# Performance work log

Hardware: AMD Instinct MI355X
Metric: run time of the kernel (lower is better)

Reference implementation:

```python
import jax, jax.numpy as jnp
import numpy as np

EMBED_DIM = 512
NUM_HEADS = 8
HEAD_DIM = EMBED_DIM // NUM_HEADS
B, S = 2, 4096


def setup_inputs() -> dict:
    key = jax.random.key(0)
    ks = jax.random.split(key, 5)
    scale = 1.0 / np.sqrt(EMBED_DIM)
    x = jax.random.normal(ks[0], (B, S, EMBED_DIM), dtype=jnp.float32)
    Wq = jax.random.normal(ks[1], (EMBED_DIM, EMBED_DIM), dtype=jnp.float32) * scale
    Wk = jax.random.normal(ks[2], (EMBED_DIM, EMBED_DIM), dtype=jnp.float32) * scale
    Wv = jax.random.normal(ks[3], (EMBED_DIM, EMBED_DIM), dtype=jnp.float32) * scale
    Wo = jax.random.normal(ks[4], (EMBED_DIM, EMBED_DIM), dtype=jnp.float32) * scale
    z = jnp.zeros((EMBED_DIM,), dtype=jnp.float32)
    return {"x": x, "Wq": Wq, "bq": z, "Wk": Wk, "bk": z, "Wv": Wv, "bv": z, "Wo": Wo, "bo": z}


def _split_heads(t):
    # [B, S, E] -> [B, H, S, Dh]
    b, s, _ = t.shape
    return t.reshape(b, s, NUM_HEADS, HEAD_DIM).transpose(0, 2, 1, 3)


def reference(x, Wq, bq, Wk, bk, Wv, bv, Wo, bo):
    q = _split_heads(x @ Wq + bq)
    k = _split_heads(x @ Wk + bk)
    v = _split_heads(x @ Wv + bv)
    # scaled dot-product attention; scale by sqrt(d_head) as in source
    scores = jnp.einsum("bhqd,bhkd->bhqk", q, k) / jnp.sqrt(jnp.float32(HEAD_DIM))
    weights = jax.nn.softmax(scores, axis=-1)
    attn = jnp.einsum("bhqk,bhkd->bhqd", weights, v)
    concat = attn.transpose(0, 2, 1, 3).reshape(x.shape[0], x.shape[1], EMBED_DIM)
    return concat @ Wo + bo
```

## Files before the change

### kernel.cpp

```cpp
#include <hip/hip_runtime.h>
#include <stdint.h>


typedef __bf16 bf16_t;
typedef bf16_t bf16x8 __attribute__((ext_vector_type(8)));
typedef float f32x4 __attribute__((ext_vector_type(4)));
typedef unsigned short u16;
typedef unsigned int u32;

__device__ __forceinline__ u16 f2bf(float f) {
  return __builtin_bit_cast(u16, (bf16_t)f);
}

__device__ __forceinline__ void gll16(const void* g, void* l) {
  __builtin_amdgcn_global_load_lds((__attribute__((address_space(1))) void*)(void*)(g),
                                   (__attribute__((address_space(3))) void*)(l), 16, 0, 0);
}

__device__ __forceinline__ float fexp2(float x) {
  float r; asm("v_exp_f32 %0, %1" : "=v"(r) : "v"(x)); return r;
}
__device__ __forceinline__ u32 cvtpk(float lo, float hi) {
  u32 r; asm("v_cvt_pk_bf16_f32 %0, %1, %2" : "=v"(r) : "v"(lo), "v"(hi)); return r;
}

__global__ void k_convert(const float* __restrict__ x, u16* __restrict__ xb, int n4) {
  int i = blockIdx.x * blockDim.x + threadIdx.x;
  if (i >= n4) return;
  float4 v = ((const float4*)x)[i];
  ushort4 o;
  o.x = f2bf(v.x); o.y = f2bf(v.y); o.z = f2bf(v.z); o.w = f2bf(v.w);
  ((ushort4*)xb)[i] = o;
}

__global__ void k_transposeW(const float* __restrict__ W0, const float* __restrict__ W1,
                             const float* __restrict__ W2, const float* __restrict__ W3,
                             u16* __restrict__ Wt) {
  __shared__ float tile[64][65];
  const float* W = (blockIdx.z == 0) ? W0 : (blockIdx.z == 1) ? W1 : (blockIdx.z == 2) ? W2 : W3;
  u16* out = Wt + (size_t)blockIdx.z * (512 * 512);
  int k0 = blockIdx.x * 64, n0 = blockIdx.y * 64;
  int t = threadIdx.x;
#pragma unroll
  for (int i = 0; i < 16; ++i) {
    int idx = i * 256 + t;
    int r = idx >> 6, c = idx & 63;
    tile[r][c] = W[(size_t)(k0 + r) * 512 + n0 + c];
  }
  __syncthreads();
#pragma unroll
  for (int i = 0; i < 16; ++i) {
    int idx = i * 256 + t;
    int n = idx >> 6, k = idx & 63;
    out[(size_t)(n0 + n) * 512 + k0 + k] = f2bf(tile[k][n]);
  }
}

__device__ __forceinline__ void gemm_core(const u16* __restrict__ A, const u16* __restrict__ Bt,
                                          int m0, int n0, uint8_t* lds, f32x4 (&acc)[4][4]) {
  int t = threadIdx.x;
  int lane = t & 63;
  int wid = t >> 6;
  int l15 = lane & 15, hib = (lane >> 4) * 16;
  int wm = wid >> 1, wn = wid & 1;
  const uint8_t* Ab = (const uint8_t*)A + (size_t)m0 * 1024;
  const uint8_t* Bb = (const uint8_t*)Bt + (size_t)n0 * 1024;

  auto STAGE = [&](int buf, int kk) {
    int kof = kk * 128;
    uint8_t* Al = lds + buf * 32768;
    uint8_t* Bl = Al + 16384;
#pragma unroll
    for (int r = 0; r < 4; ++r) {
      int L = r * 4096 + t * 16;
      int row = L >> 7;
      int colU = (L & 127) ^ ((row & 7) << 4);
      gll16(Ab + (size_t)row * 1024 + kof + colU, Al + L);
      gll16(Bb + (size_t)row * 1024 + kof + colU, Bl + L);
    }
  };

  STAGE(0, 0);
  asm volatile("s_waitcnt vmcnt(0)" ::: "memory");
  __builtin_amdgcn_s_barrier();

  int cur = 0;
  for (int kk = 0; kk < 8; ++kk) {
    if (kk + 1 < 8) STAGE(cur ^ 1, kk + 1);
    const uint8_t* Al = lds + cur * 32768;
    const uint8_t* Bl = Al + 16384;
#pragma unroll
    for (int ks = 0; ks < 2; ++ks) {
      bf16x8 af[4], bfr[4];
#pragma unroll
      for (int mi = 0; mi < 4; ++mi) {
        int row = wm * 64 + mi * 16 + l15;
        af[mi] = *(const bf16x8*)(Al + row * 128 + ((ks * 64 + hib) ^ ((row & 7) << 4)));
      }
#pragma unroll
      for (int ni = 0; ni < 4; ++ni) {
        int row = wn * 64 + ni * 16 + l15;
        bfr[ni] = *(const bf16x8*)(Bl + row * 128 + ((ks * 64 + hib) ^ ((row & 7) << 4)));
      }
#pragma unroll
      for (int mi = 0; mi < 4; ++mi)
#pragma unroll
        for (int ni = 0; ni < 4; ++ni)
          acc[mi][ni] = __builtin_amdgcn_mfma_f32_16x16x32_bf16(af[mi], bfr[ni], acc[mi][ni], 0, 0, 0);
    }
    asm volatile("s_waitcnt vmcnt(0)" ::: "memory");
    __builtin_amdgcn_s_barrier();
    cur ^= 1;
  }
}

__global__ __launch_bounds__(256, 2) void k_gemm_qkv(
    const u16* __restrict__ A, const u16* __restrict__ Wt,
    const float* __restrict__ bq, const float* __restrict__ bk, const float* __restrict__ bv,
    u16* __restrict__ Qo, u16* __restrict__ Ko, u16* __restrict__ Vt) {
  __shared__ uint8_t lds[65536];
  int z = blockIdx.z;
  const u16* Bt = Wt + (size_t)z * (512 * 512);
  const float* bias = (z == 0) ? bq : (z == 1) ? bk : bv;
  float qsc = (z == 0) ? 0.18033688011112042f : 1.0f;
  int m0 = blockIdx.y * 128, n0 = blockIdx.x * 128;
  int t = threadIdx.x, lane = t & 63, wid = t >> 6;
  int l15 = lane & 15;
  int wm = wid >> 1, wn = wid & 1;

  f32x4 acc[4][4] = {};
  gemm_core(A, Bt, m0, n0, lds, acc);

  if (z != 2) {
    u16* out = (z == 0) ? Qo : Ko;
#pragma unroll
    for (int mi = 0; mi < 4; ++mi)
#pragma unroll
      for (int ni = 0; ni < 4; ++ni) {
        int c = wn * 64 + ni * 16 + l15;
        float bsv = bias[n0 + c];
        int rbase = wm * 64 + mi * 16 + (lane >> 4) * 4;
#pragma unroll
        for (int i = 0; i < 4; ++i)
          *(u16*)(lds + (rbase + i) * 256 + c * 2) = f2bf((acc[mi][ni][i] + bsv) * qsc);
      }
    __syncthreads();
#pragma unroll
    for (int rr = 0; rr < 8; ++rr) {
      int L = rr * 4096 + t * 16;
      int row = L >> 8, col = L & 255;
      *(uint4*)((uint8_t*)out + (size_t)(m0 + row) * 1024 + n0 * 2 + col) = *(const uint4*)(lds + L);
    }
  } else {
#pragma unroll
    for (int mi = 0; mi < 4; ++mi)
#pragma unroll
      for (int ni = 0; ni < 4; ++ni) {
        int c = wn * 64 + ni * 16 + l15;
        float bsv = bias[n0 + c];
        int rbase = wm * 64 + mi * 16 + (lane >> 4) * 4;
#pragma unroll
        for (int i = 0; i < 4; ++i)
          *(u16*)(lds + c * 272 + (rbase + i) * 2) = f2bf(acc[mi][ni][i] + bsv);
      }
    __syncthreads();
    int b = m0 >> 12, s0 = m0 & 4095;
#pragma unroll
    for (int rr = 0; rr < 8; ++rr) {
      int L = rr * 4096 + t * 16;
      int cidx = L >> 8, rb = L & 255;
      *(uint4*)((uint8_t*)Vt + (size_t)(b * 512 + n0 + cidx) * 8192 + s0 * 2 + rb) =
          *(const uint4*)(lds + cidx * 272 + rb);
    }
  }
}

__global__ __launch_bounds__(256, 2) void k_gemm_out(
    const u16* __restrict__ A, const u16* __restrict__ Bt,
    const float* __restrict__ bias, float* __restrict__ out) {
  __shared__ uint8_t lds[65536];
  int m0 = blockIdx.y * 128, n0 = blockIdx.x * 128;
  int t = threadIdx.x, lane = t & 63, wid = t >> 6;
  int l15 = lane & 15;
  int wm = wid >> 1, wn = wid & 1;

  f32x4 acc[4][4] = {};
  gemm_core(A, Bt, m0, n0, lds, acc);

#pragma unroll
  for (int mi = 0; mi < 4; ++mi)
#pragma unroll
    for (int ni = 0; ni < 4; ++ni) {
      int c = wn * 64 + ni * 16 + l15;
      float bsv = bias[n0 + c];
      int rbase = wm * 64 + mi * 16 + (lane >> 4) * 4;
#pragma unroll
      for (int i = 0; i < 4; ++i)
        out[(size_t)(m0 + rbase + i) * 512 + n0 + c] = acc[mi][ni][i] + bsv;
    }
}

__global__ __launch_bounds__(256, 2) void k_attn(
    const u16* __restrict__ Q, const u16* __restrict__ K,
    const u16* __restrict__ Vt, u16* __restrict__ O) {
  __shared__ uint8_t lds[65536];
  int t = threadIdx.x, lane = t & 63, wid = t >> 6;
  int l15 = lane & 15, hi = lane >> 4;
  int g = wid >> 1, p = wid & 1;
  int bh = blockIdx.y, b = bh >> 3, h = bh & 7;
  int q0 = blockIdx.x * 128 + g * 64;

  const uint8_t* Kbase = (const uint8_t*)K + (size_t)(b * 4096) * 1024 + h * 128;
  const uint8_t* Vbase = (const uint8_t*)Vt + (size_t)(b * 512 + h * 64) * 8192;

  bf16x8 qf[4][2];
#pragma unroll
  for (int qs = 0; qs < 4; ++qs)
#pragma unroll
    for (int ks = 0; ks < 2; ++ks)
      qf[qs][ks] = *(const bf16x8*)(Q + (size_t)(b * 4096 + q0 + qs * 16 + l15) * 512 +
                                    h * 64 + ks * 32 + hi * 8);

  uint4 ou; ou.x = 0x3F803F80u; ou.y = 0x3F803F80u; ou.z = 0x3F803F80u; ou.w = 0x3F803F80u;
  const bf16x8 ones = __builtin_bit_cast(bf16x8, ou);

  f32x4 o[4][4] = {};
  f32x4 oden[4] = {};

  auto STAGE = [&](int buf, int kt2) {
    uint8_t* Kl = lds + buf * 32768;
    uint8_t* Vl = Kl + 16384;
    int kv0 = kt2 * 128;
#pragma unroll
    for (int r = 0; r < 4; ++r) {
      int L = r * 4096 + t * 16;
      int rowK = L >> 7;
      int colK = (L & 127) ^ ((rowK & 7) << 4);
      gll16(Kbase + (size_t)(kv0 + rowK) * 1024 + colK, Kl + L);
      int rowV = (L >> 7) & 63, sub = L >> 13;
      int colV = (L & 127) ^ ((rowV & 7) << 4);
      gll16(Vbase + (size_t)rowV * 8192 + (size_t)(kv0 + sub * 64) * 2 + colV, Vl + L);
    }
  };

  STAGE(0, 0);
  asm volatile("s_waitcnt vmcnt(0)" ::: "memory");
  __builtin_amdgcn_s_barrier();

  int cur = 0;
  for (int kt2 = 0; kt2 < 32; ++kt2) {
    if (kt2 + 1 < 32) STAGE(cur ^ 1, kt2 + 1);

    uint8_t* Kbuf = lds + cur * 32768;
    uint8_t* Vbuf = Kbuf + 16384;

#pragma unroll
    for (int sub = 0; sub < 2; ++sub) {
      const uint8_t* Kl = Kbuf + sub * 8192;
      const uint8_t* Vl = Vbuf + sub * 8192;

      bf16x8 kA[2][2];
#pragma unroll
      for (int ks = 0; ks < 2; ++ks)
#pragma unroll
        for (int cg = 0; cg < 2; ++cg) {
          int row = p * 32 + cg * 16 + l15;
          kA[ks][cg] = *(const bf16x8*)(Kl + row * 128 + ((ks * 64 + hi * 16) ^ ((row & 7) << 4)));
        }

      f32x4 s[4][2] = {};
      __builtin_amdgcn_s_setprio(1);
#pragma unroll
      for (int qs = 0; qs < 4; ++qs)
#pragma unroll
        for (int ks = 0; ks < 2; ++ks)
#pragma unroll
          for (int cg = 0; cg < 2; ++cg)
            s[qs][cg] = __builtin_amdgcn_mfma_f32_16x16x32_bf16(kA[ks][cg], qf[qs][ks], s[qs][cg], 0, 0, 0);
      __builtin_amdgcn_s_setprio(0);

      bf16x8 pb[4];
#pragma unroll
      for (int qs = 0; qs < 4; ++qs) {
        float pv[8];
#pragma unroll
        for (int cg = 0; cg < 2; ++cg)
#pragma unroll
          for (int i = 0; i < 4; ++i)
            pv[cg * 4 + i] = fexp2(s[qs][cg][i]);
        uint4 pu;
        pu.x = cvtpk(pv[0], pv[1]);
        pu.y = cvtpk(pv[2], pv[3]);
        pu.z = cvtpk(pv[4], pv[5]);
        pu.w = cvtpk(pv[6], pv[7]);
        pb[qs] = __builtin_bit_cast(bf16x8, pu);
      }

      __builtin_amdgcn_s_setprio(1);
#pragma unroll
      for (int qs = 0; qs < 4; ++qs)
        oden[qs] = __builtin_amdgcn_mfma_f32_16x16x32_bf16(ones, pb[qs], oden[qs], 0, 0, 0);
#pragma unroll
      for (int dg = 0; dg < 4; ++dg) {
        int row = dg * 16 + l15;
        int sw = (row & 7) << 4;
        uint2 a0 = *(const uint2*)(Vl + row * 128 + ((p * 64 + hi * 8) ^ sw));
        uint2 a1 = *(const uint2*)(Vl + row * 128 + ((p * 64 + 32 + hi * 8) ^ sw));
        uint4 vv; vv.x = a0.x; vv.y = a0.y; vv.z = a1.x; vv.w = a1.y;
        bf16x8 va = __builtin_bit_cast(bf16x8, vv);
#pragma unroll
        for (int qs = 0; qs < 4; ++qs)
          o[qs][dg] = __builtin_amdgcn_mfma_f32_16x16x32_bf16(va, pb[qs], o[qs][dg], 0, 0, 0);
      }
      __builtin_amdgcn_s_setprio(0);
    }

    asm volatile("s_waitcnt vmcnt(0)" ::: "memory");
    __builtin_amdgcn_s_barrier();
    cur ^= 1;
  }

  float den[4];
#pragma unroll
  for (int qs = 0; qs < 4; ++qs) den[qs] = oden[qs][0];

  uint8_t* base = lds + g * 17408;
  if (p) {
#pragma unroll
    for (int qs = 0; qs < 4; ++qs) {
#pragma unroll
      for (int dg = 0; dg < 4; ++dg)
        *(f32x4*)(base + ((qs * 4 + dg) * 64 + lane) * 16) = o[qs][dg];
      *(float*)(base + 16384 + (qs * 64 + lane) * 4) = den[qs];
    }
  }
  __syncthreads();
  if (!p) {
#pragma unroll
    for (int qs = 0; qs < 4; ++qs) {
      float pl = *(const float*)(base + 16384 + (qs * 64 + lane) * 4);
      float inv = 1.0f / (den[qs] + pl);
#pragma unroll
      for (int dg = 0; dg < 4; ++dg) {
        f32x4 po = *(const f32x4*)(base + ((qs * 4 + dg) * 64 + lane) * 16);
        ushort4 pk;
        pk.x = f2bf((o[qs][dg][0] + po[0]) * inv);
        pk.y = f2bf((o[qs][dg][1] + po[1]) * inv);
        pk.z = f2bf((o[qs][dg][2] + po[2]) * inv);
        pk.w = f2bf((o[qs][dg][3] + po[3]) * inv);
        *(uint2*)(O + (size_t)(b * 4096 + q0 + qs * 16 + l15) * 512 + h * 64 + dg * 16 + hi * 4) =
            __builtin_bit_cast(uint2, pk);
      }
    }
  }
}

extern "C" void kernel_launch(void* const* d_in, const int* in_sizes, int n_in,
                              void* d_out, int out_size, void* d_ws, size_t ws_size,
                              hipStream_t stream) {
  const float* x  = (const float*)d_in[0];
  const float* Wq = (const float*)d_in[1];
  const float* bq = (const float*)d_in[2];
  const float* Wk = (const float*)d_in[3];
  const float* bk = (const float*)d_in[4];
  const float* Wv = (const float*)d_in[5];
  const float* bv = (const float*)d_in[6];
  const float* Wo = (const float*)d_in[7];
  const float* bo = (const float*)d_in[8];
  float* out = (float*)d_out;

  uint8_t* ws = (uint8_t*)d_ws;
  u16* xb  = (u16*)(ws);
  u16* Wt  = (u16*)(ws + 8388608);
  u16* Qb  = (u16*)(ws + 10485760);
  u16* Kb  = (u16*)(ws + 18874368);
  u16* Vtb = (u16*)(ws + 27262976);
  u16* attn = xb;

  k_convert<<<4096, 256, 0, stream>>>(x, xb, 1048576);
  k_transposeW<<<dim3(8, 8, 4), 256, 0, stream>>>(Wq, Wk, Wv, Wo, Wt);
  k_gemm_qkv<<<dim3(4, 64, 3), 256, 0, stream>>>(xb, Wt, bq, bk, bv, Qb, Kb, Vtb);
  k_attn<<<dim3(32, 16), 256, 0, stream>>>(Qb, Kb, Vtb, attn);
  k_gemm_out<<<dim3(4, 64), 256, 0, stream>>>(attn, Wt + 3 * 262144, bo, out);
}
```

Before: 114.8 us.

## Split KV across four waves per 64-query block and load V directly from global

The attention kernel now gives each block 64 queries, and its four waves split each 128-key tile into 32-key slices. Only K is staged in LDS, which halves LDS use and raises the launch-bounds occupancy target to three blocks per CU. V is read straight from global memory in a permuted sequence order, and the QKV GEMM writes V^T with a matching position permutation so each lane's 8 contiguous values line up with the MFMA P layout. The four partial outputs are combined by a serial chain of LDS reductions across waves. The trade-offs are more global V traffic without LDS reuse and extra barriers in the epilogue, in exchange for more blocks and better occupancy.

```diff
diff --git a/kernel.cpp b/kernel.cpp
--- a/kernel.cpp
+++ b/kernel.cpp
@@ -160,8 +160,12 @@
         float bsv = bias[n0 + c];
         int rbase = wm * 64 + mi * 16 + (lane >> 4) * 4;
 #pragma unroll
-        for (int i = 0; i < 4; ++i)
-          *(u16*)(lds + c * 272 + (rbase + i) * 2) = f2bf(acc[mi][ni][i] + bsv);
+        for (int i = 0; i < 4; ++i) {
+          int sl = rbase + i;
+          int t5 = sl & 31;
+          int pos = (sl & ~31) | (t5 & 3) | (((t5 >> 4) & 1) << 2) | (((t5 >> 2) & 3) << 3);
+          *(u16*)(lds + c * 272 + pos * 2) = f2bf(acc[mi][ni][i] + bsv);
+        }
       }
     __syncthreads();
     int b = m0 >> 12, s0 = m0 & 4095;
@@ -200,15 +204,15 @@
     }
 }
 
-__global__ __launch_bounds__(256, 2) void k_attn(
+__global__ __launch_bounds__(256, 3) void k_attn(
     const u16* __restrict__ Q, const u16* __restrict__ K,
     const u16* __restrict__ Vt, u16* __restrict__ O) {
-  __shared__ uint8_t lds[65536];
+  __shared__ uint8_t lds[32768];
   int t = threadIdx.x, lane = t & 63, wid = t >> 6;
   int l15 = lane & 15, hi = lane >> 4;
-  int g = wid >> 1, p = wid & 1;
+  int p = wid;
   int bh = blockIdx.y, b = bh >> 3, h = bh & 7;
-  int q0 = blockIdx.x * 128 + g * 64;
+  int q0 = blockIdx.x * 64;
 
   const uint8_t* Kbase = (const uint8_t*)K + (size_t)(b * 4096) * 1024 + h * 128;
   const uint8_t* Vbase = (const uint8_t*)Vt + (size_t)(b * 512 + h * 64) * 8192;
@@ -228,18 +232,14 @@
   f32x4 oden[4] = {};
 
   auto STAGE = [&](int buf, int kt2) {
-    uint8_t* Kl = lds + buf * 32768;
-    uint8_t* Vl = Kl + 16384;
+    uint8_t* Kl = lds + buf * 16384;
     int kv0 = kt2 * 128;
 #pragma unroll
     for (int r = 0; r < 4; ++r) {
       int L = r * 4096 + t * 16;
-      int rowK = L >> 7;
-      int colK = (L & 127) ^ ((rowK & 7) << 4);
-      gll16(Kbase + (size_t)(kv0 + rowK) * 1024 + colK, Kl + L);
-      int rowV = (L >> 7) & 63, sub = L >> 13;
-      int colV = (L & 127) ^ ((rowV & 7) << 4);
-      gll16(Vbase + (size_t)rowV * 8192 + (size_t)(kv0 + sub * 64) * 2 + colV, Vl + L);
+      int row = L >> 7;
+      int col = (L & 127) ^ ((row & 7) << 4);
+      gll16(Kbase + (size_t)(kv0 + row) * 1024 + col, Kl + L);
     }
   };
 
@@ -251,69 +251,61 @@
   for (int kt2 = 0; kt2 < 32; ++kt2) {
     if (kt2 + 1 < 32) STAGE(cur ^ 1, kt2 + 1);
 
-    uint8_t* Kbuf = lds + cur * 32768;
-    uint8_t* Vbuf = Kbuf + 16384;
-
-#pragma unroll
-    for (int sub = 0; sub < 2; ++sub) {
-      const uint8_t* Kl = Kbuf + sub * 8192;
-      const uint8_t* Vl = Vbuf + sub * 8192;
-
-      bf16x8 kA[2][2];
+    const uint8_t* Kl = lds + cur * 16384;
+
+    size_t kvb = (size_t)(kt2 * 128 + p * 32 + hi * 8) * 2;
+    bf16x8 va[4];
+#pragma unroll
+    for (int dg = 0; dg < 4; ++dg)
+      va[dg] = *(const bf16x8*)(Vbase + (size_t)(dg * 16 + l15) * 8192 + kvb);
+
+    bf16x8 kA[2][2];
+#pragma unroll
+    for (int ks = 0; ks < 2; ++ks)
+#pragma unroll
+      for (int cg = 0; cg < 2; ++cg) {
+        int row = p * 32 + cg * 16 + l15;
+        kA[ks][cg] = *(const bf16x8*)(Kl + row * 128 + ((ks * 64 + hi * 16) ^ ((row & 7) << 4)));
+      }
+
+    f32x4 s[4][2] = {};
+    __builtin_amdgcn_s_setprio(1);
+#pragma unroll
+    for (int qs = 0; qs < 4; ++qs)
 #pragma unroll
       for (int ks = 0; ks < 2; ++ks)
 #pragma unroll
-        for (int cg = 0; cg < 2; ++cg) {
-          int row = p * 32 + cg * 16 + l15;
-          kA[ks][cg] = *(const bf16x8*)(Kl + row * 128 + ((ks * 64 + hi * 16) ^ ((row & 7) << 4)));
-        }
-
-      f32x4 s[4][2] = {};
-      __builtin_amdgcn_s_setprio(1);
+        for (int cg = 0; cg < 2; ++cg)
+          s[qs][cg] = __builtin_amdgcn_mfma_f32_16x16x32_bf16(kA[ks][cg], qf[qs][ks], s[qs][cg], 0, 0, 0);
+    __builtin_amdgcn_s_setprio(0);
+
+    bf16x8 pb[4];
+#pragma unroll
+    for (int qs = 0; qs < 4; ++qs) {
+      float pv[8];
+#pragma unroll
+      for (int cg = 0; cg < 2; ++cg)
+#pragma unroll
+        for (int i = 0; i < 4; ++i)
+          pv[cg * 4 + i] = fexp2(s[qs][cg][i]);
+      uint4 pu;
+      pu.x = cvtpk(pv[0], pv[1]);
+      pu.y = cvtpk(pv[2], pv[3]);
+      pu.z = cvtpk(pv[4], pv[5]);
+      pu.w = cvtpk(pv[6], pv[7]);
+      pb[qs] = __builtin_bit_cast(bf16x8, pu);
+    }
+
+    __builtin_amdgcn_s_setprio(1);
+#pragma unroll
+    for (int qs = 0; qs < 4; ++qs)
+      oden[qs] = __builtin_amdgcn_mfma_f32_16x16x32_bf16(ones, pb[qs], oden[qs], 0, 0, 0);
+#pragma unroll
+    for (int dg = 0; dg < 4; ++dg)
 #pragma unroll
       for (int qs = 0; qs < 4; ++qs)
-#pragma unroll
-        for (int ks = 0; ks < 2; ++ks)
-#pragma unroll
-          for (int cg = 0; cg < 2; ++cg)
-            s[qs][cg] = __builtin_amdgcn_mfma_f32_16x16x32_bf16(kA[ks][cg], qf[qs][ks], s[qs][cg], 0, 0, 0);
-      __builtin_amdgcn_s_setprio(0);
-
-      bf16x8 pb[4];
-#pragma unroll
-      for (int qs = 0; qs < 4; ++qs) {
-        float pv[8];
-#pragma unroll
-        for (int cg = 0; cg < 2; ++cg)
-#pragma unroll
-          for (int i = 0; i < 4; ++i)
-            pv[cg * 4 + i] = fexp2(s[qs][cg][i]);
-        uint4 pu;
-        pu.x = cvtpk(pv[0], pv[1]);
-        pu.y = cvtpk(pv[2], pv[3]);
-        pu.z = cvtpk(pv[4], pv[5]);
-        pu.w = cvtpk(pv[6], pv[7]);
-        pb[qs] = __builtin_bit_cast(bf16x8, pu);
-      }
-
-      __builtin_amdgcn_s_setprio(1);
-#pragma unroll
-      for (int qs = 0; qs < 4; ++qs)
-        oden[qs] = __builtin_amdgcn_mfma_f32_16x16x32_bf16(ones, pb[qs], oden[qs], 0, 0, 0);
-#pragma unroll
-      for (int dg = 0; dg < 4; ++dg) {
-        int row = dg * 16 + l15;
-        int sw = (row & 7) << 4;
-        uint2 a0 = *(const uint2*)(Vl + row * 128 + ((p * 64 + hi * 8) ^ sw));
-        uint2 a1 = *(const uint2*)(Vl + row * 128 + ((p * 64 + 32 + hi * 8) ^ sw));
-        uint4 vv; vv.x = a0.x; vv.y = a0.y; vv.z = a1.x; vv.w = a1.y;
-        bf16x8 va = __builtin_bit_cast(bf16x8, vv);
-#pragma unroll
-        for (int qs = 0; qs < 4; ++qs)
-          o[qs][dg] = __builtin_amdgcn_mfma_f32_16x16x32_bf16(va, pb[qs], o[qs][dg], 0, 0, 0);
-      }
-      __builtin_amdgcn_s_setprio(0);
-    }
+        o[qs][dg] = __builtin_amdgcn_mfma_f32_16x16x32_bf16(va[dg], pb[qs], o[qs][dg], 0, 0, 0);
+    __builtin_amdgcn_s_setprio(0);
 
     asm volatile("s_waitcnt vmcnt(0)" ::: "memory");
     __builtin_amdgcn_s_barrier();
@@ -324,30 +316,43 @@
 #pragma unroll
   for (int qs = 0; qs < 4; ++qs) den[qs] = oden[qs][0];
 
-  uint8_t* base = lds + g * 17408;
-  if (p) {
+  auto store_p = [&]() {
 #pragma unroll
     for (int qs = 0; qs < 4; ++qs) {
 #pragma unroll
       for (int dg = 0; dg < 4; ++dg)
-        *(f32x4*)(base + ((qs * 4 + dg) * 64 + lane) * 16) = o[qs][dg];
-      *(float*)(base + 16384 + (qs * 64 + lane) * 4) = den[qs];
-    }
-  }
+        *(f32x4*)(lds + ((qs * 4 + dg) * 64 + lane) * 16) = o[qs][dg];
+      *(float*)(lds + 16384 + (qs * 64 + lane) * 4) = den[qs];
+    }
+  };
+  auto load_add = [&]() {
+#pragma unroll
+    for (int qs = 0; qs < 4; ++qs) {
+#pragma unroll
+      for (int dg = 0; dg < 4; ++dg)
+        o[qs][dg] += *(const f32x4*)(lds + ((qs * 4 + dg) * 64 + lane) * 16);
+      den[qs] += *(const float*)(lds + 16384 + (qs * 64 + lane) * 4);
+    }
+  };
+
+  if (wid == 3) store_p();
   __syncthreads();
-  if (!p) {
+  if (wid == 2) { load_add(); store_p(); }
+  __syncthreads();
+  if (wid == 1) { load_add(); store_p(); }
+  __syncthreads();
+  if (wid == 0) {
+    load_add();
 #pragma unroll
     for (int qs = 0; qs < 4; ++qs) {
-      float pl = *(const float*)(base + 16384 + (qs * 64 + lane) * 4);
-      float inv = 1.0f / (den[qs] + pl);
+      float inv = 1.0f / den[qs];
 #pragma unroll
       for (int dg = 0; dg < 4; ++dg) {
-        f32x4 po = *(const f32x4*)(base + ((qs * 4 + dg) * 64 + lane) * 16);
         ushort4 pk;
-        pk.x = f2bf((o[qs][dg][0] + po[0]) * inv);
-        pk.y = f2bf((o[qs][dg][1] + po[1]) * inv);
-        pk.z = f2bf((o[qs][dg][2] + po[2]) * inv);
-        pk.w = f2bf((o[qs][dg][3] + po[3]) * inv);
+        pk.x = f2bf(o[qs][dg][0] * inv);
+        pk.y = f2bf(o[qs][dg][1] * inv);
+        pk.z = f2bf(o[qs][dg][2] * inv);
+        pk.w = f2bf(o[qs][dg][3] * inv);
         *(uint2*)(O + (size_t)(b * 4096 + q0 + qs * 16 + l15) * 512 + h * 64 + dg * 16 + hi * 4) =
             __builtin_bit_cast(uint2, pk);
       }
@@ -380,6 +385,6 @@
   k_convert<<<4096, 256, 0, stream>>>(x, xb, 1048576);
   k_transposeW<<<dim3(8, 8, 4), 256, 0, stream>>>(Wq, Wk, Wv, Wo, Wt);
   k_gemm_qkv<<<dim3(4, 64, 3), 256, 0, stream>>>(xb, Wt, bq, bk, bv, Qb, Kb, Vtb);
-  k_attn<<<dim3(32, 16), 256, 0, stream>>>(Qb, Kb, Vtb, attn);
+  k_attn<<<dim3(64, 16), 256, 0, stream>>>(Qb, Kb, Vtb, attn);
   k_gemm_out<<<dim3(4, 64), 256, 0, stream>>>(attn, Wt + 3 * 262144, bo, out);
 }
```

Result: slower. 209.7 us (+82.7%).

## Pre-permute V layout in projection epilogue and load V fragments directly from global

Applied to the files above, without the earlier changes.

The QKV projection epilogue now writes V into a blocked, pre-permuted layout: 32-key blocks per head, with the row order inside each block shuffled to match the MFMA operand order. This lets the attention kernel load each V fragment straight from global memory as one 16-byte vector load per lane, instead of staging V through LDS with swizzled reads. The aim is to halve LDS use (65536 to 34816 bytes) and cut the LDS staging and ds_read traffic for V, which could allow more resident blocks. In exchange, V loads now go to global/L2 inside the inner loop without software prefetch, so their latency may be exposed.

```diff
diff --git a/kernel.cpp b/kernel.cpp
--- a/kernel.cpp
+++ b/kernel.cpp
@@ -160,8 +160,12 @@
         float bsv = bias[n0 + c];
         int rbase = wm * 64 + mi * 16 + (lane >> 4) * 4;
 #pragma unroll
-        for (int i = 0; i < 4; ++i)
-          *(u16*)(lds + c * 272 + (rbase + i) * 2) = f2bf(acc[mi][ni][i] + bsv);
+        for (int i = 0; i < 4; ++i) {
+          int sl = rbase + i;
+          int t5 = sl & 31;
+          int pos = (sl & ~31) | (t5 & 3) | (((t5 >> 4) & 1) << 2) | (((t5 >> 2) & 3) << 3);
+          *(u16*)(lds + c * 272 + pos * 2) = f2bf(acc[mi][ni][i] + bsv);
+        }
       }
     __syncthreads();
     int b = m0 >> 12, s0 = m0 & 4095;
@@ -169,7 +173,9 @@
     for (int rr = 0; rr < 8; ++rr) {
       int L = rr * 4096 + t * 16;
       int cidx = L >> 8, rb = L & 255;
-      *(uint4*)((uint8_t*)Vt + (size_t)(b * 512 + n0 + cidx) * 8192 + s0 * 2 + rb) =
+      int e = n0 + cidx, h = e >> 6, d = e & 63;
+      int kb = (s0 >> 5) + (rb >> 6);
+      *(uint4*)((uint8_t*)Vt + ((size_t)(b * 8 + h) * 128 + kb) * 4096 + d * 64 + (rb & 63)) =
           *(const uint4*)(lds + cidx * 272 + rb);
     }
   }
@@ -203,7 +209,7 @@
 __global__ __launch_bounds__(256, 2) void k_attn(
     const u16* __restrict__ Q, const u16* __restrict__ K,
     const u16* __restrict__ Vt, u16* __restrict__ O) {
-  __shared__ uint8_t lds[65536];
+  __shared__ uint8_t lds[34816];
   int t = threadIdx.x, lane = t & 63, wid = t >> 6;
   int l15 = lane & 15, hi = lane >> 4;
   int g = wid >> 1, p = wid & 1;
@@ -211,7 +217,7 @@
   int q0 = blockIdx.x * 128 + g * 64;
 
   const uint8_t* Kbase = (const uint8_t*)K + (size_t)(b * 4096) * 1024 + h * 128;
-  const uint8_t* Vbase = (const uint8_t*)Vt + (size_t)(b * 512 + h * 64) * 8192;
+  const uint8_t* Vbase = (const uint8_t*)Vt + (size_t)(b * 8 + h) * 524288;
 
   bf16x8 qf[4][2];
 #pragma unroll
@@ -228,18 +234,14 @@
   f32x4 oden[4] = {};
 
   auto STAGE = [&](int buf, int kt2) {
-    uint8_t* Kl = lds + buf * 32768;
-    uint8_t* Vl = Kl + 16384;
+    uint8_t* Kl = lds + buf * 16384;
     int kv0 = kt2 * 128;
 #pragma unroll
     for (int r = 0; r < 4; ++r) {
       int L = r * 4096 + t * 16;
-      int rowK = L >> 7;
-      int colK = (L & 127) ^ ((rowK & 7) << 4);
-      gll16(Kbase + (size_t)(kv0 + rowK) * 1024 + colK, Kl + L);
-      int rowV = (L >> 7) & 63, sub = L >> 13;
-      int colV = (L & 127) ^ ((rowV & 7) << 4);
-      gll16(Vbase + (size_t)rowV * 8192 + (size_t)(kv0 + sub * 64) * 2 + colV, Vl + L);
+      int row = L >> 7;
+      int col = (L & 127) ^ ((row & 7) << 4);
+      gll16(Kbase + (size_t)(kv0 + row) * 1024 + col, Kl + L);
     }
   };
 
@@ -251,13 +253,17 @@
   for (int kt2 = 0; kt2 < 32; ++kt2) {
     if (kt2 + 1 < 32) STAGE(cur ^ 1, kt2 + 1);
 
-    uint8_t* Kbuf = lds + cur * 32768;
-    uint8_t* Vbuf = Kbuf + 16384;
+    const uint8_t* Kbuf = lds + cur * 16384;
 
 #pragma unroll
     for (int sub = 0; sub < 2; ++sub) {
       const uint8_t* Kl = Kbuf + sub * 8192;
-      const uint8_t* Vl = Vbuf + sub * 8192;
+
+      int kb = kt2 * 4 + sub * 2 + p;
+      bf16x8 va[4];
+#pragma unroll
+      for (int dg = 0; dg < 4; ++dg)
+        va[dg] = *(const bf16x8*)(Vbase + (size_t)kb * 4096 + (dg * 16 + l15) * 64 + hi * 16);
 
       bf16x8 kA[2][2];
 #pragma unroll
@@ -301,17 +307,10 @@
       for (int qs = 0; qs < 4; ++qs)
         oden[qs] = __builtin_amdgcn_mfma_f32_16x16x32_bf16(ones, pb[qs], oden[qs], 0, 0, 0);
 #pragma unroll
-      for (int dg = 0; dg < 4; ++dg) {
-        int row = dg * 16 + l15;
-        int sw = (row & 7) << 4;
-        uint2 a0 = *(const uint2*)(Vl + row * 128 + ((p * 64 + hi * 8) ^ sw));
-        uint2 a1 = *(const uint2*)(Vl + row * 128 + ((p * 64 + 32 + hi * 8) ^ sw));
-        uint4 vv; vv.x = a0.x; vv.y = a0.y; vv.z = a1.x; vv.w = a1.y;
-        bf16x8 va = __builtin_bit_cast(bf16x8, vv);
+      for (int dg = 0; dg < 4; ++dg)
 #pragma unroll
         for (int qs = 0; qs < 4; ++qs)
-          o[qs][dg] = __builtin_amdgcn_mfma_f32_16x16x32_bf16(va, pb[qs], o[qs][dg], 0, 0, 0);
-      }
+          o[qs][dg] = __builtin_amdgcn_mfma_f32_16x16x32_bf16(va[dg], pb[qs], o[qs][dg], 0, 0, 0);
       __builtin_amdgcn_s_setprio(0);
     }
 
```

New measurement: 117.2 us. 1.02x slower.

## Single-buffer GEMM LDS for higher occupancy and stage output stores through LDS

Applied to the files above, without the earlier changes.

The GEMM core drops the double-buffered LDS pipeline in favour of one 32KB stage with barriers around each load, cutting shared memory from 64KB to about 34KB so three blocks fit per CU (launch bounds raised to 3). The output GEMM epilogue now writes accumulators into padded LDS in two halves and then emits coalesced float4 global stores instead of scattered scalar stores. The trade is that global-load latency is no longer hidden by prefetch inside a block and must be covered by the extra resident blocks instead.

```diff
diff --git a/kernel.cpp b/kernel.cpp
--- a/kernel.cpp
+++ b/kernel.cpp
@@ -65,42 +65,30 @@
   int wm = wid >> 1, wn = wid & 1;
   const uint8_t* Ab = (const uint8_t*)A + (size_t)m0 * 1024;
   const uint8_t* Bb = (const uint8_t*)Bt + (size_t)n0 * 1024;
-
-  auto STAGE = [&](int buf, int kk) {
+  for (int kk = 0; kk < 8; ++kk) {
+    __syncthreads();
     int kof = kk * 128;
-    uint8_t* Al = lds + buf * 32768;
-    uint8_t* Bl = Al + 16384;
 #pragma unroll
     for (int r = 0; r < 4; ++r) {
       int L = r * 4096 + t * 16;
       int row = L >> 7;
       int colU = (L & 127) ^ ((row & 7) << 4);
-      gll16(Ab + (size_t)row * 1024 + kof + colU, Al + L);
-      gll16(Bb + (size_t)row * 1024 + kof + colU, Bl + L);
-    }
-  };
-
-  STAGE(0, 0);
-  asm volatile("s_waitcnt vmcnt(0)" ::: "memory");
-  __builtin_amdgcn_s_barrier();
-
-  int cur = 0;
-  for (int kk = 0; kk < 8; ++kk) {
-    if (kk + 1 < 8) STAGE(cur ^ 1, kk + 1);
-    const uint8_t* Al = lds + cur * 32768;
-    const uint8_t* Bl = Al + 16384;
+      gll16(Ab + (size_t)row * 1024 + kof + colU, lds + L);
+      gll16(Bb + (size_t)row * 1024 + kof + colU, lds + 16384 + L);
+    }
+    __syncthreads();
 #pragma unroll
     for (int ks = 0; ks < 2; ++ks) {
       bf16x8 af[4], bfr[4];
 #pragma unroll
       for (int mi = 0; mi < 4; ++mi) {
         int row = wm * 64 + mi * 16 + l15;
-        af[mi] = *(const bf16x8*)(Al + row * 128 + ((ks * 64 + hib) ^ ((row & 7) << 4)));
+        af[mi] = *(const bf16x8*)(lds + row * 128 + ((ks * 64 + hib) ^ ((row & 7) << 4)));
       }
 #pragma unroll
       for (int ni = 0; ni < 4; ++ni) {
         int row = wn * 64 + ni * 16 + l15;
-        bfr[ni] = *(const bf16x8*)(Bl + row * 128 + ((ks * 64 + hib) ^ ((row & 7) << 4)));
+        bfr[ni] = *(const bf16x8*)(lds + 16384 + row * 128 + ((ks * 64 + hib) ^ ((row & 7) << 4)));
       }
 #pragma unroll
       for (int mi = 0; mi < 4; ++mi)
@@ -108,17 +96,15 @@
         for (int ni = 0; ni < 4; ++ni)
           acc[mi][ni] = __builtin_amdgcn_mfma_f32_16x16x32_bf16(af[mi], bfr[ni], acc[mi][ni], 0, 0, 0);
     }
-    asm volatile("s_waitcnt vmcnt(0)" ::: "memory");
-    __builtin_amdgcn_s_barrier();
-    cur ^= 1;
-  }
-}
-
-__global__ __launch_bounds__(256, 2) void k_gemm_qkv(
+  }
+  __syncthreads();
+}
+
+__global__ __launch_bounds__(256, 3) void k_gemm_qkv(
     const u16* __restrict__ A, const u16* __restrict__ Wt,
     const float* __restrict__ bq, const float* __restrict__ bk, const float* __restrict__ bv,
     u16* __restrict__ Qo, u16* __restrict__ Ko, u16* __restrict__ Vt) {
-  __shared__ uint8_t lds[65536];
+  __shared__ uint8_t lds[34816];
   int z = blockIdx.z;
   const u16* Bt = Wt + (size_t)z * (512 * 512);
   const float* bias = (z == 0) ? bq : (z == 1) ? bk : bv;
@@ -175,10 +161,10 @@
   }
 }
 
-__global__ __launch_bounds__(256, 2) void k_gemm_out(
+__global__ __launch_bounds__(256, 3) void k_gemm_out(
     const u16* __restrict__ A, const u16* __restrict__ Bt,
     const float* __restrict__ bias, float* __restrict__ out) {
-  __shared__ uint8_t lds[65536];
+  __shared__ uint8_t lds[34816];
   int m0 = blockIdx.y * 128, n0 = blockIdx.x * 128;
   int t = threadIdx.x, lane = t & 63, wid = t >> 6;
   int l15 = lane & 15;
@@ -188,16 +174,30 @@
   gemm_core(A, Bt, m0, n0, lds, acc);
 
 #pragma unroll
-  for (int mi = 0; mi < 4; ++mi)
-#pragma unroll
-    for (int ni = 0; ni < 4; ++ni) {
-      int c = wn * 64 + ni * 16 + l15;
-      float bsv = bias[n0 + c];
-      int rbase = wm * 64 + mi * 16 + (lane >> 4) * 4;
-#pragma unroll
-      for (int i = 0; i < 4; ++i)
-        out[(size_t)(m0 + rbase + i) * 512 + n0 + c] = acc[mi][ni][i] + bsv;
-    }
+  for (int half = 0; half < 2; ++half) {
+    __syncthreads();
+    if (wm == half) {
+#pragma unroll
+      for (int mi = 0; mi < 4; ++mi)
+#pragma unroll
+        for (int ni = 0; ni < 4; ++ni) {
+          int c = wn * 64 + ni * 16 + l15;
+          float bsv = bias[n0 + c];
+          int rbase = mi * 16 + (lane >> 4) * 4;
+#pragma unroll
+          for (int i = 0; i < 4; ++i)
+            *(float*)(lds + (rbase + i) * 528 + c * 4) = acc[mi][ni][i] + bsv;
+        }
+    }
+    __syncthreads();
+#pragma unroll
+    for (int it = 0; it < 8; ++it) {
+      int idx = it * 256 + t;
+      int row = idx >> 5, c16 = idx & 31;
+      *(float4*)(out + (size_t)(m0 + half * 64 + row) * 512 + n0 + c16 * 4) =
+          *(const float4*)(lds + row * 528 + c16 * 16);
+    }
+  }
 }
 
 __global__ __launch_bounds__(256, 2) void k_attn(
```

After: 115.1 us. Within noise of the previous version (+0.3%).
